# Kernel tuning notes

Measured on AMD Instinct MI355X. Metric: run time of the kernel, lower is better.

Reference implementation:

```python
import jax, jax.numpy as jnp
import numpy as np

N_NODES = 100000
NEG_SLOPE = 0.01  # F.leaky_relu default


def setup_inputs() -> dict:
    key = jax.random.key(0)
    k1, k2, k3, k4, k5 = jax.random.split(key, 5)
    x = jax.random.normal(k1, (N_NODES, 128), dtype=jnp.float32)
    edge_index = jax.random.randint(k2, (2, 1600000), 0, N_NODES, dtype=jnp.int64)
    # GCNConv linear weights (PyG: x @ W.T), bias added after aggregation
    W1 = jax.random.normal(k3, (128, 128), dtype=jnp.float32) * (1.0 / np.sqrt(128))
    b1 = jnp.zeros((128,), dtype=jnp.float32)
    W2 = jax.random.normal(k4, (128, 128), dtype=jnp.float32) * (1.0 / np.sqrt(128))
    b2 = jnp.zeros((128,), dtype=jnp.float32)
    return {"x": x, "edge_index": edge_index, "W1": W1, "b1": b1, "W2": W2, "b2": b2}


def _gcn_layer(x, W, b, src, dst, norm, self_w):
    # linear transform first (GCNConv order): h = x @ W.T
    h = x @ W.T
    # message passing: sum_j norm_ij * h_j  (edges) + self-loop term h_i / deg_i
    msg = h[src] * norm[:, None]                       # [E, F] gather (memory-bound)
    agg = jax.ops.segment_sum(msg, dst, num_segments=x.shape[0])
    out = agg + h * self_w[:, None] + b
    return out


def reference(x, edge_index, W1, b1, W2, b2):
    src = edge_index[0]
    dst = edge_index[1]
    n = x.shape[0]
    # gcn_norm with self-loops: deg_i = in-degree(dst) + 1
    deg = jax.ops.segment_sum(jnp.ones_like(dst, dtype=x.dtype), dst, num_segments=n) + 1.0
    deg_inv_sqrt = jax.lax.rsqrt(deg)
    norm = deg_inv_sqrt[src] * deg_inv_sqrt[dst]       # edge weights
    self_w = deg_inv_sqrt * deg_inv_sqrt               # self-loop weight = 1/deg

    h = _gcn_layer(x, W1, b1, src, dst, norm, self_w)
    h = jax.nn.leaky_relu(h, NEG_SLOPE)
    # dropout inactive (eval semantics)
    h = _gcn_layer(h, W2, b2, src, dst, norm, self_w)
    h = jax.nn.leaky_relu(h, NEG_SLOPE)
    return h
```

## Files before the change

kernel.cpp:

```cpp
#include <hip/hip_runtime.h>

#define F 128
#define NEG_SLOPE 0.01f
#define NPB 256
#define PMAX 512
#define HB 4096
#define BB 8192
#define CAP 6144

typedef _Float16 half8_t __attribute__((ext_vector_type(8)));
typedef float f32x4 __attribute__((ext_vector_type(4)));


__global__ __launch_bounds__(512) void zero_bcnt(int* __restrict__ bcnt) {
    bcnt[threadIdx.x] = 0;
}

__global__ __launch_bounds__(256) void hist_kernel(const int* __restrict__ dst,
                                                   int* __restrict__ bcnt,
                                                   int E, int nP) {
    __shared__ int h[PMAX];
    int tid = threadIdx.x;
    for (int i = tid; i < nP; i += 256) h[i] = 0;
    __syncthreads();
    int base = blockIdx.x * HB;
    for (int i = tid; i < HB && base + i < E; i += 256)
        atomicAdd(&h[dst[base + i] >> 8], 1);
    __syncthreads();
    for (int i = tid; i < nP; i += 256)
        if (h[i]) atomicAdd(&bcnt[i], h[i]);
}

__global__ __launch_bounds__(512) void scan_bk(const int* __restrict__ bcnt,
                                               int* __restrict__ bbase,
                                               int* __restrict__ bcur, int nP) {
    __shared__ int s[512];
    int tid = threadIdx.x;
    int v = (tid < nP) ? bcnt[tid] : 0;
    int run = v;
    s[tid] = v;
    __syncthreads();
    for (int off = 1; off < 512; off <<= 1) {
        int add = (tid >= off) ? s[tid - off] : 0;
        __syncthreads();
        run += add;
        s[tid] = run;
        __syncthreads();
    }
    if (tid < nP) { bbase[tid] = run - v; bcur[tid] = run - v; }
}

__global__ __launch_bounds__(256) void bin_kernel(const int* __restrict__ src,
                                                  const int* __restrict__ dst,
                                                  int* __restrict__ bcur,
                                                  int* __restrict__ binned,
                                                  int E, int nP) {
    __shared__ int hist[PMAX];
    __shared__ int lbase[PMAX];
    __shared__ int gbase[PMAX];
    __shared__ int cur[PMAX];
    __shared__ int sa[PMAX];
    __shared__ int buf[BB];
    __shared__ unsigned short b16[BB];
    int tid = threadIdx.x;
    int base = blockIdx.x * BB;
    int myE = E - base; if (myE > BB) myE = BB;

    for (int i = tid; i < nP; i += 256) hist[i] = 0;
    __syncthreads();
    for (int i = tid; i < myE; i += 256)
        atomicAdd(&hist[dst[base + i] >> 8], 1);
    __syncthreads();
    {
        int j0 = tid, j1 = tid + 256;
        sa[j0] = (j0 < nP) ? hist[j0] : 0;
        sa[j1] = (j1 < nP) ? hist[j1] : 0;
        __syncthreads();
        for (int off = 1; off < PMAX; off <<= 1) {
            int t0 = sa[j0] + (j0 >= off ? sa[j0 - off] : 0);
            int t1 = sa[j1] + (j1 >= off ? sa[j1 - off] : 0);
            __syncthreads();
            sa[j0] = t0; sa[j1] = t1;
            __syncthreads();
        }
        if (j0 < nP) { lbase[j0] = sa[j0] - hist[j0]; cur[j0] = sa[j0] - hist[j0]; }
        if (j1 < nP) { lbase[j1] = sa[j1] - hist[j1]; cur[j1] = sa[j1] - hist[j1]; }
    }
    __syncthreads();
    for (int i = tid; i < nP; i += 256)
        gbase[i] = hist[i] ? atomicAdd(&bcur[i], hist[i]) : 0;
    __syncthreads();
    for (int i = tid; i < myE; i += 256) {
        int d = dst[base + i], s = src[base + i];
        int b = d >> 8;
        int lp = atomicAdd(&cur[b], 1);
        buf[lp] = ((d & (NPB - 1)) << 17) | s;
        b16[lp] = (unsigned short)b;
    }
    __syncthreads();
    for (int j = tid; j < myE; j += 256) {
        int b = b16[j];
        binned[gbase[b] + (j - lbase[b])] = buf[j];
    }
}

__global__ __launch_bounds__(256) void csr_kernel(const int* __restrict__ binned,
                                                  const int* __restrict__ bcnt,
                                                  const int* __restrict__ bbase,
                                                  int* __restrict__ srcs,
                                                  int* __restrict__ offs,
                                                  float* __restrict__ dis, int N) {
    __shared__ int cnt[NPB];
    __shared__ int tmp[NPB];
    __shared__ int cur[NPB];
    __shared__ int buf[CAP];
    int tid = threadIdx.x;
    int b = blockIdx.x;
    int ebase = bbase[b];
    int count = bcnt[b];
    int lo = b << 8;
    cnt[tid] = 0;
    __syncthreads();
    for (int j = tid; j < count; j += 256)
        atomicAdd(&cnt[binned[ebase + j] >> 17], 1);
    __syncthreads();
    int v = cnt[tid];
    int run = v;
    tmp[tid] = v;
    __syncthreads();
    for (int off = 1; off < 256; off <<= 1) {
        int add = (tid >= off) ? tmp[tid - off] : 0;
        __syncthreads();
        run += add;
        tmp[tid] = run;
        __syncthreads();
    }
    int excl = run - v;
    cur[tid] = excl;
    int node = lo + tid;
    if (node < N) {
        offs[node] = ebase + excl;
        dis[node] = rsqrtf((float)v + 1.0f);
    }
    __syncthreads();
    for (int j = tid; j < count; j += 256) {
        int rec = binned[ebase + j];
        int pos = atomicAdd(&cur[rec >> 17], 1);
        int s = rec & 0x1FFFF;
        if (pos < CAP) buf[pos] = s; else srcs[ebase + pos] = s;
    }
    __syncthreads();
    int lim = count < CAP ? count : CAP;
    for (int j = tid; j < lim; j += 256)
        srcs[ebase + j] = buf[j];
}


__global__ __launch_bounds__(256) void cvt_w(const float* __restrict__ W1,
                                             const float* __restrict__ W2,
                                             _Float16* __restrict__ W1h,
                                             _Float16* __restrict__ W2h) {
    int i = blockIdx.x * 256 + threadIdx.x;
    const int n4 = F * F / 4;
    const float* in = (i < n4) ? W1 : W2;
    _Float16* out = (i < n4) ? W1h : W2h;
    int j = (i < n4) ? i : i - n4;
    float4 v = ((const float4*)in)[j];
    half8_t h;
    h[0] = (_Float16)v.x; h[1] = (_Float16)v.y;
    h[2] = (_Float16)v.z; h[3] = (_Float16)v.w;
    *(int2*)&((_Float16*)out)[j * 4] = *(int2*)&h;
}


__device__ __forceinline__ void gemm_core(const half8_t afrag[4],
                                          const _Float16* __restrict__ Wh,
                                          int m, int quad,
                                          _Float16* __restrict__ orow) {
    f32x4 acc[8];
#pragma unroll
    for (int t = 0; t < 8; ++t) acc[t] = (f32x4){0.f, 0.f, 0.f, 0.f};
#pragma unroll
    for (int c = 0; c < 4; ++c) {
#pragma unroll
        for (int t = 0; t < 8; ++t) {
            half8_t bfrag = *(const half8_t*)&Wh[(t * 16 + m) * F + c * 32 + quad * 8];
            acc[t] = __builtin_amdgcn_mfma_f32_16x16x32_f16(afrag[c], bfrag, acc[t],
                                                            0, 0, 0);
        }
    }
#pragma unroll
    for (int t = 0; t < 8; ++t)
#pragma unroll
        for (int r = 0; r < 4; ++r)
            orow[(quad * 4 + r) * F + t * 16 + m] = (_Float16)acc[t][r];
}

__global__ __launch_bounds__(256) void gemm_a32(const float* __restrict__ A,
                                                const _Float16* __restrict__ Wh,
                                                _Float16* __restrict__ out,
                                                int ntiles) {
    int wave = threadIdx.x >> 6;
    int lane = threadIdx.x & 63;
    int tile = blockIdx.x * 4 + wave;
    if (tile >= ntiles) return;
    int m = lane & 15, quad = lane >> 4;
    const float* arow = A + (size_t)tile * 16 * F;
    half8_t afrag[4];
#pragma unroll
    for (int c = 0; c < 4; ++c) {
        float4 t0 = *(const float4*)&arow[m * F + c * 32 + quad * 8];
        float4 t1 = *(const float4*)&arow[m * F + c * 32 + quad * 8 + 4];
        afrag[c][0] = (_Float16)t0.x; afrag[c][1] = (_Float16)t0.y;
        afrag[c][2] = (_Float16)t0.z; afrag[c][3] = (_Float16)t0.w;
        afrag[c][4] = (_Float16)t1.x; afrag[c][5] = (_Float16)t1.y;
        afrag[c][6] = (_Float16)t1.z; afrag[c][7] = (_Float16)t1.w;
    }
    gemm_core(afrag, Wh, m, quad, out + (size_t)tile * 16 * F);
}

__global__ __launch_bounds__(256) void gemm_a16(const _Float16* __restrict__ A,
                                                const _Float16* __restrict__ Wh,
                                                _Float16* __restrict__ out,
                                                int ntiles) {
    int wave = threadIdx.x >> 6;
    int lane = threadIdx.x & 63;
    int tile = blockIdx.x * 4 + wave;
    if (tile >= ntiles) return;
    int m = lane & 15, quad = lane >> 4;
    const _Float16* arow = A + (size_t)tile * 16 * F;
    half8_t afrag[4];
#pragma unroll
    for (int c = 0; c < 4; ++c)
        afrag[c] = *(const half8_t*)&arow[m * F + c * 32 + quad * 8];
    gemm_core(afrag, Wh, m, quad, out + (size_t)tile * 16 * F);
}


#define AGG_BODY(H8)                                                           \
    int node = blockIdx.x * 4 + (threadIdx.x >> 6);                            \
    int lane = threadIdx.x & 63;                                               \
    if (node >= n) return;                                                     \
    int g = lane >> 4;                                                         \
    int fo = lane & 15;                                                        \
    int beg = offs[node];                                                      \
    int end = (node + 1 < n) ? offs[node + 1] : E;                             \
    float acc[8];                                                              \
    _Pragma("unroll") for (int j = 0; j < 8; ++j) acc[j] = 0.f;                \
    for (int e = beg; e < end; e += 8) {                                       \
        int i0 = e + g, i1 = e + 4 + g;                                        \
        int s0 = srcs[i0 < end ? i0 : end - 1];                                \
        int s1 = srcs[i1 < end ? i1 : end - 1];                                \
        float w0 = (i0 < end) ? dis[s0] : 0.f;                                 \
        float w1 = (i1 < end) ? dis[s1] : 0.f;                                 \
        half8_t a0 = H8[(size_t)s0 * 16 + fo];                                 \
        half8_t a1 = H8[(size_t)s1 * 16 + fo];                                 \
        _Pragma("unroll") for (int j = 0; j < 8; ++j)                          \
            acc[j] += w0 * (float)a0[j] + w1 * (float)a1[j];                   \
    }                                                                          \
    _Pragma("unroll") for (int j = 0; j < 8; ++j) {                            \
        acc[j] += __shfl_xor(acc[j], 16);                                      \
        acc[j] += __shfl_xor(acc[j], 32);                                      \
    }                                                                          \
    if (lane >= 16) return;                                                    \
    float di = dis[node];                                                      \
    float sw = di * di;                                                        \
    half8_t hv = H8[(size_t)node * 16 + fo];                                   \
    float4 b0 = ((const float4*)bias)[fo * 2];                                 \
    float4 b1v = ((const float4*)bias)[fo * 2 + 1];                            \
    acc[0] = di * acc[0] + sw * (float)hv[0] + b0.x;                           \
    acc[1] = di * acc[1] + sw * (float)hv[1] + b0.y;                           \
    acc[2] = di * acc[2] + sw * (float)hv[2] + b0.z;                           \
    acc[3] = di * acc[3] + sw * (float)hv[3] + b0.w;                           \
    acc[4] = di * acc[4] + sw * (float)hv[4] + b1v.x;                          \
    acc[5] = di * acc[5] + sw * (float)hv[5] + b1v.y;                          \
    acc[6] = di * acc[6] + sw * (float)hv[6] + b1v.z;                          \
    acc[7] = di * acc[7] + sw * (float)hv[7] + b1v.w;                          \
    _Pragma("unroll") for (int j = 0; j < 8; ++j)                              \
        acc[j] = (acc[j] > 0.f) ? acc[j] : acc[j] * NEG_SLOPE;

__global__ __launch_bounds__(256) void agg_to_h(const half8_t* __restrict__ h8,
                                                const float* __restrict__ dis,
                                                const float* __restrict__ bias,
                                                const int* __restrict__ srcs,
                                                const int* __restrict__ offs,
                                                half8_t* __restrict__ out,
                                                int n, int E) {
    AGG_BODY(h8)
    half8_t o;
#pragma unroll
    for (int j = 0; j < 8; ++j) o[j] = (_Float16)acc[j];
    out[(size_t)node * 16 + fo] = o;
}

__global__ __launch_bounds__(256) void agg_to_f(const half8_t* __restrict__ h8,
                                                const float* __restrict__ dis,
                                                const float* __restrict__ bias,
                                                const int* __restrict__ srcs,
                                                const int* __restrict__ offs,
                                                float* __restrict__ out,
                                                int n, int E) {
    AGG_BODY(h8)
    float4 o0 = make_float4(acc[0], acc[1], acc[2], acc[3]);
    float4 o1 = make_float4(acc[4], acc[5], acc[6], acc[7]);
    ((float4*)out)[(size_t)node * 32 + fo * 2] = o0;
    ((float4*)out)[(size_t)node * 32 + fo * 2 + 1] = o1;
}


static inline size_t alup(size_t x) { return (x + 255) & ~(size_t)255; }

extern "C" void kernel_launch(void* const* d_in, const int* in_sizes, int n_in,
                              void* d_out, int out_size, void* d_ws, size_t ws_size,
                              hipStream_t stream) {
    const float* x  = (const float*)d_in[0];
    const int*   ei = (const int*)d_in[1];
    const float* W1 = (const float*)d_in[2];
    const float* b1 = (const float*)d_in[3];
    const float* W2 = (const float*)d_in[4];
    const float* b2 = (const float*)d_in[5];
    float* out = (float*)d_out;

    const int N = in_sizes[0] / F;
    const int E = in_sizes[1] / 2;
    const int* src = ei;
    const int* dst = ei + E;

    char* p = (char*)d_ws;
    int*      bcnt   = (int*)p;      p += alup(PMAX * 4);
    int*      bbase  = (int*)p;      p += alup(PMAX * 4);
    int*      bcur   = (int*)p;      p += alup(PMAX * 4);
    float*    dis    = (float*)p;    p += alup((size_t)N * 4);
    int*      offs   = (int*)p;      p += alup((size_t)N * 4);
    int*      binned = (int*)p;      p += alup((size_t)E * 4);
    int*      srcs   = (int*)p;      p += alup((size_t)E * 4);
    _Float16* g      = (_Float16*)p; p += alup((size_t)N * F * 2);
    _Float16* hh     = (_Float16*)p; p += alup((size_t)N * F * 2);
    _Float16* W1h    = (_Float16*)p; p += alup((size_t)F * F * 2);
    _Float16* W2h    = (_Float16*)p; p += alup((size_t)F * F * 2);

    const int nP = (N + NPB - 1) / NPB;
    const int ntiles = (N + 15) / 16;
    const int gemm_grid = (ntiles + 3) / 4;

    zero_bcnt<<<1, 512, 0, stream>>>(bcnt);
    hist_kernel<<<(E + HB - 1) / HB, 256, 0, stream>>>(dst, bcnt, E, nP);
    scan_bk<<<1, 512, 0, stream>>>(bcnt, bbase, bcur, nP);
    bin_kernel<<<(E + BB - 1) / BB, 256, 0, stream>>>(src, dst, bcur, binned, E, nP);
    csr_kernel<<<nP, 256, 0, stream>>>(binned, bcnt, bbase, srcs, offs, dis, N);
    cvt_w<<<(2 * F * F / 4 + 255) / 256, 256, 0, stream>>>(W1, W2, W1h, W2h);

    gemm_a32<<<gemm_grid, 256, 0, stream>>>(x, W1h, hh, ntiles);
    agg_to_h<<<(N + 3) / 4, 256, 0, stream>>>((const half8_t*)hh, dis, b1, srcs,
                                              offs, (half8_t*)g, N, E);
    gemm_a16<<<gemm_grid, 256, 0, stream>>>(g, W2h, hh, ntiles);
    agg_to_f<<<(N + 3) / 4, 256, 0, stream>>>((const half8_t*)hh, dis, b2, srcs,
                                              offs, out, N, E);
}
```

Baseline: 365.7 us.

## Pre-scale GEMM outputs by source norm and prefetch edge indices in aggregation

Measured after the change: 342.0 us. -6.5%, faster.

```diff
diff --git a/kernel.cpp b/kernel.cpp
--- a/kernel.cpp
+++ b/kernel.cpp
@@ -175,7 +175,8 @@
 
 __device__ __forceinline__ void gemm_core(const half8_t afrag[4],
                                           const _Float16* __restrict__ Wh,
-                                          int m, int quad,
+                                          const float* __restrict__ dis,
+                                          int tile, int m, int quad,
                                           _Float16* __restrict__ orow) {
     f32x4 acc[8];
 #pragma unroll
@@ -189,15 +190,19 @@
                                                             0, 0, 0);
         }
     }
+    float d[4];
+#pragma unroll
+    for (int r = 0; r < 4; ++r) d[r] = dis[tile * 16 + quad * 4 + r];
 #pragma unroll
     for (int t = 0; t < 8; ++t)
 #pragma unroll
         for (int r = 0; r < 4; ++r)
-            orow[(quad * 4 + r) * F + t * 16 + m] = (_Float16)acc[t][r];
+            orow[(quad * 4 + r) * F + t * 16 + m] = (_Float16)(acc[t][r] * d[r]);
 }
 
 __global__ __launch_bounds__(256) void gemm_a32(const float* __restrict__ A,
                                                 const _Float16* __restrict__ Wh,
+                                                const float* __restrict__ dis,
                                                 _Float16* __restrict__ out,
                                                 int ntiles) {
     int wave = threadIdx.x >> 6;
@@ -216,11 +221,12 @@
         afrag[c][4] = (_Float16)t1.x; afrag[c][5] = (_Float16)t1.y;
         afrag[c][6] = (_Float16)t1.z; afrag[c][7] = (_Float16)t1.w;
     }
-    gemm_core(afrag, Wh, m, quad, out + (size_t)tile * 16 * F);
+    gemm_core(afrag, Wh, dis, tile, m, quad, out + (size_t)tile * 16 * F);
 }
 
 __global__ __launch_bounds__(256) void gemm_a16(const _Float16* __restrict__ A,
                                                 const _Float16* __restrict__ Wh,
+                                                const float* __restrict__ dis,
                                                 _Float16* __restrict__ out,
                                                 int ntiles) {
     int wave = threadIdx.x >> 6;
@@ -233,7 +239,7 @@
 #pragma unroll
     for (int c = 0; c < 4; ++c)
         afrag[c] = *(const half8_t*)&arow[m * F + c * 32 + quad * 8];
-    gemm_core(afrag, Wh, m, quad, out + (size_t)tile * 16 * F);
+    gemm_core(afrag, Wh, dis, tile, m, quad, out + (size_t)tile * 16 * F);
 }
 
 
@@ -247,16 +253,28 @@
     int end = (node + 1 < n) ? offs[node + 1] : E;                             \
     float acc[8];                                                              \
     _Pragma("unroll") for (int j = 0; j < 8; ++j) acc[j] = 0.f;                \
-    for (int e = beg; e < end; e += 8) {                                       \
-        int i0 = e + g, i1 = e + 4 + g;                                        \
-        int s0 = srcs[i0 < end ? i0 : end - 1];                                \
-        int s1 = srcs[i1 < end ? i1 : end - 1];                                \
-        float w0 = (i0 < end) ? dis[s0] : 0.f;                                 \
-        float w1 = (i1 < end) ? dis[s1] : 0.f;                                 \
-        half8_t a0 = H8[(size_t)s0 * 16 + fo];                                 \
-        half8_t a1 = H8[(size_t)s1 * 16 + fo];                                 \
-        _Pragma("unroll") for (int j = 0; j < 8; ++j)                          \
-            acc[j] += w0 * (float)a0[j] + w1 * (float)a1[j];                   \
+    if (beg < end) {                                                           \
+        int i0 = beg + g, i1 = beg + 4 + g;                                    \
+        int s0 = srcs[i0 < end ? i0 : beg];                                    \
+        int s1 = srcs[i1 < end ? i1 : beg];                                    \
+        float w0 = (i0 < end) ? 1.f : 0.f;                                     \
+        float w1 = (i1 < end) ? 1.f : 0.f;                                     \
+        for (int e = beg; e < end; e += 8) {                                   \
+            int ns0 = s0, ns1 = s1;                                            \
+            float nw0 = 0.f, nw1 = 0.f;                                        \
+            if (e + 8 < end) {                                                 \
+                int j0 = e + 8 + g, j1 = e + 12 + g;                           \
+                ns0 = srcs[j0 < end ? j0 : beg];                               \
+                ns1 = srcs[j1 < end ? j1 : beg];                               \
+                nw0 = (j0 < end) ? 1.f : 0.f;                                  \
+                nw1 = (j1 < end) ? 1.f : 0.f;                                  \
+            }                                                                  \
+            half8_t a0 = H8[(size_t)s0 * 16 + fo];                             \
+            half8_t a1 = H8[(size_t)s1 * 16 + fo];                             \
+            _Pragma("unroll") for (int j = 0; j < 8; ++j)                      \
+                acc[j] += w0 * (float)a0[j] + w1 * (float)a1[j];               \
+            s0 = ns0; s1 = ns1; w0 = nw0; w1 = nw1;                            \
+        }                                                                      \
     }                                                                          \
     _Pragma("unroll") for (int j = 0; j < 8; ++j) {                            \
         acc[j] += __shfl_xor(acc[j], 16);                                      \
@@ -264,18 +282,17 @@
     }                                                                          \
     if (lane >= 16) return;                                                    \
     float di = dis[node];                                                      \
-    float sw = di * di;                                                        \
     half8_t hv = H8[(size_t)node * 16 + fo];                                   \
     float4 b0 = ((const float4*)bias)[fo * 2];                                 \
     float4 b1v = ((const float4*)bias)[fo * 2 + 1];                            \
-    acc[0] = di * acc[0] + sw * (float)hv[0] + b0.x;                           \
-    acc[1] = di * acc[1] + sw * (float)hv[1] + b0.y;                           \
-    acc[2] = di * acc[2] + sw * (float)hv[2] + b0.z;                           \
-    acc[3] = di * acc[3] + sw * (float)hv[3] + b0.w;                           \
-    acc[4] = di * acc[4] + sw * (float)hv[4] + b1v.x;                          \
-    acc[5] = di * acc[5] + sw * (float)hv[5] + b1v.y;                          \
-    acc[6] = di * acc[6] + sw * (float)hv[6] + b1v.z;                          \
-    acc[7] = di * acc[7] + sw * (float)hv[7] + b1v.w;                          \
+    acc[0] = di * (acc[0] + (float)hv[0]) + b0.x;                              \
+    acc[1] = di * (acc[1] + (float)hv[1]) + b0.y;                              \
+    acc[2] = di * (acc[2] + (float)hv[2]) + b0.z;                              \
+    acc[3] = di * (acc[3] + (float)hv[3]) + b0.w;                              \
+    acc[4] = di * (acc[4] + (float)hv[4]) + b1v.x;                             \
+    acc[5] = di * (acc[5] + (float)hv[5]) + b1v.y;                             \
+    acc[6] = di * (acc[6] + (float)hv[6]) + b1v.z;                             \
+    acc[7] = di * (acc[7] + (float)hv[7]) + b1v.w;                             \
     _Pragma("unroll") for (int j = 0; j < 8; ++j)                              \
         acc[j] = (acc[j] > 0.f) ? acc[j] : acc[j] * NEG_SLOPE;
 
@@ -350,10 +367,10 @@
     csr_kernel<<<nP, 256, 0, stream>>>(binned, bcnt, bbase, srcs, offs, dis, N);
     cvt_w<<<(2 * F * F / 4 + 255) / 256, 256, 0, stream>>>(W1, W2, W1h, W2h);
 
-    gemm_a32<<<gemm_grid, 256, 0, stream>>>(x, W1h, hh, ntiles);
+    gemm_a32<<<gemm_grid, 256, 0, stream>>>(x, W1h, dis, hh, ntiles);
     agg_to_h<<<(N + 3) / 4, 256, 0, stream>>>((const half8_t*)hh, dis, b1, srcs,
                                               offs, (half8_t*)g, N, E);
-    gemm_a16<<<gemm_grid, 256, 0, stream>>>(g, W2h, hh, ntiles);
+    gemm_a16<<<gemm_grid, 256, 0, stream>>>(g, W2h, dis, hh, ntiles);
     agg_to_f<<<(N + 3) / 4, 256, 0, stream>>>((const half8_t*)hh, dis, b2, srcs,
                                               offs, out, N, E);
 }
```
